# Performance work log

Measured on AMD Instinct MI355X. Metric: run time of the kernel, lower is better.

The kernel has to match this reference:

```python
import jax, jax.numpy as jnp
import numpy as np

N_NODES = 50000
N_EDGES = 800000
D_IN, D_HID, N_CLS, N_PROT = 128, 256, 16, 512
EPS = 1e-6


def setup_inputs() -> dict:
    key = jax.random.key(0)
    ks = jax.random.split(key, 12)
    s = 0.05
    return {
        "x": jax.random.normal(ks[0], (N_NODES, D_IN), dtype=jnp.float32),
        "edge_index": jax.random.randint(ks[1], (2, N_EDGES), 0, N_NODES, dtype=jnp.int64),
        "prot": jax.random.randint(ks[2], (N_PROT,), 0, N_NODES, dtype=jnp.int64),
        "epoch": 1,
        "W0": jax.random.normal(ks[3], (D_IN, D_HID), dtype=jnp.float32) * s,
        "b0": jnp.zeros((D_HID,), jnp.float32),
        "W1": jax.random.normal(ks[4], (D_HID, D_HID), dtype=jnp.float32) * s,
        "b1": jnp.zeros((D_HID,), jnp.float32),
        "Wl1": jax.random.normal(ks[5], (D_HID, D_HID), dtype=jnp.float32) * s,
        "bl1": jnp.zeros((D_HID,), jnp.float32),
        "Wl2": jax.random.normal(ks[6], (D_HID, N_CLS), dtype=jnp.float32) * s,
        "bl2": jnp.zeros((N_CLS,), jnp.float32),
    }


def _gcn_layer(h, W, b, src, dst, norm, n):
    # PyG GCNConv: h' = scatter_add(norm * (h @ W)[src] -> dst) + b
    m = (h @ W)[src] * norm[:, None]
    return jax.ops.segment_sum(m, dst, num_segments=n) + b


def _forward(x, edge_index, prot, W0, b0, W1, b1, Wl1, bl1, Wl2, bl2):
    n = x.shape[0]
    loops = jnp.arange(n, dtype=edge_index.dtype)
    src = jnp.concatenate([edge_index[0], loops])
    dst = jnp.concatenate([edge_index[1], loops])
    deg = jax.ops.segment_sum(jnp.ones_like(dst, dtype=x.dtype), dst, num_segments=n)
    dis = jax.lax.rsqrt(deg)  # deg >= 1 thanks to self loops
    norm = dis[src] * dis[dst]

    h = jax.nn.relu(_gcn_layer(x, W0, b0, src, dst, norm, n))
    h = _gcn_layer(h, W1, b1, src, dst, norm, n)

    # L2 row-normalize (torch divides by the norm directly)
    qn = jnp.linalg.norm(h, axis=1, keepdims=True)
    h = h / qn

    # relative_rep: cosine similarity of every node to each anchor
    anchors = h[prot]                             # [P, H]
    nx = jnp.linalg.norm(h, axis=1)               # [N]
    na = jnp.linalg.norm(anchors, axis=1)         # [P]
    num = h @ anchors.T                           # [N, P]
    x_rel = num / jnp.maximum(nx[:, None] * na[None, :], EPS)

    # classifier head on prototypes -> out_proto, then composed prediction
    lin = lambda z: jax.nn.relu(z @ Wl1 + bl1) @ Wl2 + bl2
    out_proto = jax.nn.log_softmax(lin(anchors), axis=-1)   # [P, C]
    out = jax.nn.log_softmax(x_rel @ out_proto, axis=-1)    # [N, C]
    return out, x_rel, out_proto


def reference(x, edge_index, prot, epoch, W0, b0, W1, b1, Wl1, bl1, Wl2, bl2):
    # epoch >= first_step_epochs (=0) branch: inference-path composition
    return _forward(x, edge_index, prot, W0, b0, W1, b1, Wl1, bl1, Wl2, bl2)


if __name__ == "__main__":
    out, x_rel, out_proto = reference(**setup_inputs())
    print(out.shape, x_rel.shape, out_proto.shape)
```

## Files before the change

kernel.cpp:

```cpp
#include <hip/hip_runtime.h>
#include <hip/hip_bf16.h>
#include <math.h>

#define NN 50000
#define NP 50048
#define EE 800000
#define DIN 128
#define HID 256
#define NCLS 16
#define NPROT 512

typedef __attribute__((ext_vector_type(8))) short short8;
typedef __attribute__((ext_vector_type(4))) float f32x4;

__device__ inline unsigned short f2b(float f) {
    union { float f; unsigned u; } c; c.f = f;
    unsigned u = c.u;
    unsigned r = (u + 0x7FFFu + ((u >> 16) & 1u)) >> 16;
    return (unsigned short)r;
}
__device__ inline float b2f(unsigned short u) {
    union { unsigned u; float f; } c; c.u = ((unsigned)u) << 16; return c.f;
}

#define GL2LDS16(g, l)                                                              \
    __builtin_amdgcn_global_load_lds(                                               \
        (const __attribute__((address_space(1))) unsigned int*)(g),                 \
        (__attribute__((address_space(3))) unsigned int*)(l), 16, 0, 0)


__global__ __launch_bounds__(256) void k_count(const int* __restrict__ dst, int* __restrict__ cnt, int e) {
    int i = blockIdx.x * 256 + threadIdx.x;
    if (i < e) atomicAdd(&cnt[dst[i]], 1);
}

__global__ __launch_bounds__(256) void k_scan1(const int* __restrict__ cnt, int* __restrict__ excl,
                                               int* __restrict__ bsum, float* __restrict__ dis, int n) {
    __shared__ int s[256];
    int t = threadIdx.x;
    int i = blockIdx.x * 256 + t;
    int v = (i < n) ? cnt[i] : 0;
    if (i < n) dis[i] = rsqrtf((float)v + 1.0f);
    s[t] = v; __syncthreads();
    for (int d = 1; d < 256; d <<= 1) {
        int add = (t >= d) ? s[t - d] : 0;
        __syncthreads();
        s[t] += add;
        __syncthreads();
    }
    if (i < n) excl[i] = s[t] - v;
    if (t == 255) bsum[blockIdx.x] = s[255];
}

__global__ __launch_bounds__(256) void k_scan2(const int* __restrict__ bsum, int* __restrict__ boff, int nb) {
    __shared__ int s[256];
    int t = threadIdx.x;
    int v = (t < nb) ? bsum[t] : 0;
    s[t] = v; __syncthreads();
    for (int d = 1; d < 256; d <<= 1) {
        int add = (t >= d) ? s[t - d] : 0;
        __syncthreads();
        s[t] += add;
        __syncthreads();
    }
    if (t < nb) boff[t] = s[t] - v;
}

__global__ __launch_bounds__(256) void k_scan3(const int* __restrict__ excl, const int* __restrict__ boff,
                                               int* __restrict__ off, int n, int e) {
    int i = blockIdx.x * 256 + threadIdx.x;
    if (i < n) off[i] = excl[i] + boff[blockIdx.x];
    if (i == 0) off[n] = e;
}

__global__ __launch_bounds__(256) void k_fill(const int* __restrict__ src, const int* __restrict__ dst,
                                              const int* __restrict__ off, int* __restrict__ cursor,
                                              const float* __restrict__ dis,
                                              int2* __restrict__ csr_e, int e) {
    int i = blockIdx.x * 256 + threadIdx.x;
    if (i >= e) return;
    int s = src[i], d = dst[i];
    int pos = atomicAdd(&cursor[d], 1);
    csr_e[off[d] + pos] = make_int2(s, __float_as_int(dis[s] * dis[d]));
}


#define CAST_BLKS (NN * DIN / 4 / 256)
#define WT0_BLKS  (DIN * HID / 256)
#define WT1_BLKS  (HID * HID / 256)

__global__ __launch_bounds__(256) void k_prep(const float* __restrict__ x, unsigned short* __restrict__ xb,
                                              const float* __restrict__ W0, unsigned short* __restrict__ Wt0,
                                              const float* __restrict__ W1, unsigned short* __restrict__ Wt1) {
    int b = blockIdx.x, t = threadIdx.x;
    if (b < CAST_BLKS) {
        int i = b * 256 + t;
        float4 v = ((const float4*)x)[i];
        ushort4 o; o.x = f2b(v.x); o.y = f2b(v.y); o.z = f2b(v.z); o.w = f2b(v.w);
        ((ushort4*)xb)[i] = o;
    } else if (b < CAST_BLKS + WT0_BLKS) {
        int i = (b - CAST_BLKS) * 256 + t;
        int k = i / HID, n = i - k * HID;
        Wt0[n * DIN + k] = f2b(W0[(size_t)k * HID + n]);
    } else {
        int i = (b - CAST_BLKS - WT0_BLKS) * 256 + t;
        int k = i / HID, n = i - k * HID;
        Wt1[n * HID + k] = f2b(W1[(size_t)k * HID + n]);
    }
}


__global__ __launch_bounds__(256) void k_gemm_mfma(const unsigned short* __restrict__ A,
                                                   const unsigned short* __restrict__ Bt,
                                                   void* __restrict__ C, int M, int Nc, int K, int mode,
                                                   const float* __restrict__ nx, const float* __restrict__ na,
                                                   const float* __restrict__ bias) {
    __shared__ __align__(16) unsigned short As[128 * 32];
    __shared__ __align__(16) unsigned short Bs[128 * 32];
    const int t = threadIdx.x;
    const int lane = t & 63;
    const int quad = lane >> 4;
    const int l16 = lane & 15;
    const int wv = t >> 6;
    const int wm = (wv & 1) * 64, wn = (wv >> 1) * 64;
    const int m0 = blockIdx.y * 128, n0 = blockIdx.x * 128;

    f32x4 acc[4][4];
#pragma unroll
    for (int i = 0; i < 4; ++i)
#pragma unroll
        for (int j = 0; j < 4; ++j)
#pragma unroll
            for (int r = 0; r < 4; ++r) acc[i][j][r] = 0.0f;

    const int sr = t >> 2;
    const int sc = (t & 3) * 8;

    for (int k0 = 0; k0 < K; k0 += 32) {
        GL2LDS16(A + (size_t)(m0 + sr) * K + k0 + sc,       &As[t * 8]);
        GL2LDS16(A + (size_t)(m0 + 64 + sr) * K + k0 + sc,  &As[2048 + t * 8]);
        GL2LDS16(Bt + (size_t)(n0 + sr) * K + k0 + sc,      &Bs[t * 8]);
        GL2LDS16(Bt + (size_t)(n0 + 64 + sr) * K + k0 + sc, &Bs[2048 + t * 8]);
        __syncthreads();
        short8 af[4], bf[4];
#pragma unroll
        for (int i = 0; i < 4; ++i)
            af[i] = *(const short8*)&As[(wm + i * 16 + l16) * 32 + quad * 8];
#pragma unroll
        for (int j = 0; j < 4; ++j)
            bf[j] = *(const short8*)&Bs[(wn + j * 16 + l16) * 32 + quad * 8];
#pragma unroll
        for (int i = 0; i < 4; ++i)
#pragma unroll
            for (int j = 0; j < 4; ++j)
                acc[i][j] = __builtin_amdgcn_mfma_f32_16x16x32_bf16(af[i], bf[j], acc[i][j], 0, 0, 0);
        __syncthreads();
    }

#pragma unroll
    for (int i = 0; i < 4; ++i) {
        int rb = m0 + wm + i * 16 + quad * 4;
#pragma unroll
        for (int j = 0; j < 4; ++j) {
            int col = n0 + wn + j * 16 + l16;
#pragma unroll
            for (int rg = 0; rg < 4; ++rg) {
                int r = rb + rg;
                float v = acc[i][j][rg];
                if (mode == 0) {
                    ((unsigned short*)C)[(size_t)r * Nc + col] = f2b(v);
                } else if (mode == 2) {
                    v = fmaxf(v + bias[col], 0.0f);
                    ((unsigned short*)C)[(size_t)r * Nc + col] = f2b(v);
                } else if (r < M) {
                    float s = fmaxf(nx[r] * na[col], 1e-6f);
                    ((float*)C)[(size_t)r * Nc + col] = v / s;
                }
            }
        }
    }
}


__global__ __launch_bounds__(256) void k_agg128(const unsigned short* __restrict__ xw, const int* __restrict__ off,
                                                const int2* __restrict__ csr, const float* __restrict__ dis,
                                                unsigned short* __restrict__ out, int n) {
    int node = (blockIdx.x * 256 + threadIdx.x) >> 6;
    int lane = threadIdx.x & 63;
    if (node >= n) return;
    float d = dis[node];
    float w0 = d * d;
    ushort2 u = ((const ushort2*)(xw + (size_t)node * DIN))[lane];
    float a0 = w0 * b2f(u.x), a1 = w0 * b2f(u.y);
    int p = off[node], p1 = off[node + 1];
#define G128(e)                                                           \
    {                                                                     \
        ushort2 v = ((const ushort2*)(xw + (size_t)(e).x * DIN))[lane];   \
        float w = __int_as_float((e).y);                                  \
        a0 = fmaf(w, b2f(v.x), a0); a1 = fmaf(w, b2f(v.y), a1);           \
    }
    for (; p + 3 < p1; p += 4) {
        int2 e0 = csr[p], e1 = csr[p + 1], e2 = csr[p + 2], e3 = csr[p + 3];
        G128(e0) G128(e1) G128(e2) G128(e3)
    }
    for (; p < p1; ++p) { int2 e0 = csr[p]; G128(e0) }
#undef G128
    ushort2 o; o.x = f2b(a0); o.y = f2b(a1);
    ((ushort2*)(out + (size_t)node * DIN))[lane] = o;
}


__global__ __launch_bounds__(256) void k_agg256(const unsigned short* __restrict__ xw, const int* __restrict__ off,
                                                const int2* __restrict__ csr, const float* __restrict__ dis,
                                                const float* __restrict__ bias,
                                                unsigned short* __restrict__ out, float* __restrict__ nx, int n) {
    int node = (blockIdx.x * 256 + threadIdx.x) >> 6;
    int lane = threadIdx.x & 63;
    if (node >= n) return;
    float d = dis[node];
    float w0 = d * d;
    ushort4 u = ((const ushort4*)(xw + (size_t)node * HID))[lane];
    float a0 = w0 * b2f(u.x), a1 = w0 * b2f(u.y), a2 = w0 * b2f(u.z), a3 = w0 * b2f(u.w);
    int p = off[node], p1 = off[node + 1];
#define G256(e)                                                           \
    {                                                                     \
        ushort4 v = ((const ushort4*)(xw + (size_t)(e).x * HID))[lane];   \
        float w = __int_as_float((e).y);                                  \
        a0 = fmaf(w, b2f(v.x), a0); a1 = fmaf(w, b2f(v.y), a1);           \
        a2 = fmaf(w, b2f(v.z), a2); a3 = fmaf(w, b2f(v.w), a3);           \
    }
    for (; p + 3 < p1; p += 4) {
        int2 e0 = csr[p], e1 = csr[p + 1], e2 = csr[p + 2], e3 = csr[p + 3];
        G256(e0) G256(e1) G256(e2) G256(e3)
    }
    for (; p < p1; ++p) { int2 e0 = csr[p]; G256(e0) }
#undef G256
    float4 b = ((const float4*)bias)[lane];
    a0 += b.x; a1 += b.y; a2 += b.z; a3 += b.w;
    float ss = a0 * a0 + a1 * a1 + a2 * a2 + a3 * a3;
    for (int m = 32; m >= 1; m >>= 1) ss += __shfl_xor(ss, m, 64);
    float qn = sqrtf(ss);
    a0 /= qn; a1 /= qn; a2 /= qn; a3 /= qn;
    float s2 = a0 * a0 + a1 * a1 + a2 * a2 + a3 * a3;
    for (int m = 32; m >= 1; m >>= 1) s2 += __shfl_xor(s2, m, 64);
    if (lane == 0) nx[node] = sqrtf(s2);
    ushort4 o; o.x = f2b(a0); o.y = f2b(a1); o.z = f2b(a2); o.w = f2b(a3);
    ((ushort4*)(out + (size_t)node * HID))[lane] = o;
}


__global__ __launch_bounds__(256) void k_gproto(const unsigned short* __restrict__ hb,
                                                const int* __restrict__ prot, const float* __restrict__ nx,
                                                unsigned short* __restrict__ aRb, float* __restrict__ na,
                                                const float* __restrict__ Wl1, const float* __restrict__ bl1,
                                                const float* __restrict__ Wl2, const float* __restrict__ bl2,
                                                float* __restrict__ outp) {
    __shared__ float sa[HID];
    __shared__ float st[HID];
    int row = blockIdx.x, t = threadIdx.x;
    int p = prot[row];
    unsigned short us = hb[(size_t)p * HID + t];
    aRb[(size_t)row * HID + t] = us;
    sa[t] = b2f(us);
    if (t == 0) na[row] = nx[p];
    __syncthreads();
    float acc = bl1[t];
#pragma unroll 8
    for (int k = 0; k < HID; ++k) acc = fmaf(sa[k], Wl1[k * HID + t], acc);
    st[t] = fmaxf(acc, 0.0f);
    __syncthreads();
    if (t < 64) {
        int c = t & 15, ch = t >> 4;
        float z = 0.f;
#pragma unroll 8
        for (int k = ch * 64; k < ch * 64 + 64; ++k) z = fmaf(st[k], Wl2[k * NCLS + c], z);
        z += __shfl_xor(z, 16, 64);
        z += __shfl_xor(z, 32, 64);
        z += bl2[c];
        float m = z;
        for (int d = 8; d >= 1; d >>= 1) m = fmaxf(m, __shfl_xor(m, d, 64));
        float e = expf(z - m);
        float s = e;
        for (int d = 8; d >= 1; d >>= 1) s += __shfl_xor(s, d, 64);
        if (t < 16) outp[row * NCLS + c] = z - m - logf(s);
    }
}


__global__ __launch_bounds__(256) void k_final(const float* __restrict__ xrel, const float* __restrict__ proto,
                                               float* __restrict__ out, int M) {
    __shared__ __align__(16) unsigned short pT[16 * 520];
    int t = threadIdx.x;
    for (int i = t; i < NPROT * NCLS; i += 256) {
        int k = i >> 4, c = i & 15;
        pT[c * 520 + k] = f2b(proto[i]);
    }
    __syncthreads();
    const int lane = t & 63, wv = t >> 6;
    const int quad = lane >> 4, l16 = lane & 15;
    short8 bfr[16];
#pragma unroll
    for (int ks = 0; ks < 16; ++ks)
        bfr[ks] = *(const short8*)&pT[l16 * 520 + ks * 32 + quad * 8];
    int m0 = blockIdx.x * 128;
#pragma unroll
    for (int mt = 0; mt < 2; ++mt) {
        int tile0 = m0 + (wv * 2 + mt) * 16;
        int r = tile0 + l16;
        int rl = (r < M) ? r : (M - 1);
        const float* xr = xrel + (size_t)rl * NPROT + quad * 8;
        f32x4 acc = {0.f, 0.f, 0.f, 0.f};
#pragma unroll
        for (int ks = 0; ks < 16; ++ks) {
            float4 v0 = *(const float4*)(xr + ks * 32);
            float4 v1 = *(const float4*)(xr + ks * 32 + 4);
            short8 af;
            af[0] = (short)f2b(v0.x); af[1] = (short)f2b(v0.y);
            af[2] = (short)f2b(v0.z); af[3] = (short)f2b(v0.w);
            af[4] = (short)f2b(v1.x); af[5] = (short)f2b(v1.y);
            af[6] = (short)f2b(v1.z); af[7] = (short)f2b(v1.w);
            acc = __builtin_amdgcn_mfma_f32_16x16x32_bf16(af, bfr[ks], acc, 0, 0, 0);
        }
#pragma unroll
        for (int rg = 0; rg < 4; ++rg) {
            int row = tile0 + quad * 4 + rg;
            float z = acc[rg];
            float mx = z;
            for (int d = 8; d >= 1; d >>= 1) mx = fmaxf(mx, __shfl_xor(mx, d, 64));
            float e = expf(z - mx);
            float s = e;
            for (int d = 8; d >= 1; d >>= 1) s += __shfl_xor(s, d, 64);
            if (row < M) out[(size_t)row * NCLS + l16] = z - mx - logf(s);
        }
    }
}


extern "C" void kernel_launch(void* const* d_in, const int* in_sizes, int n_in,
                              void* d_out, int out_size, void* d_ws, size_t ws_size,
                              hipStream_t stream) {
    const float* x    = (const float*)d_in[0];
    const int*   eidx = (const int*)d_in[1];
    const int*   prot = (const int*)d_in[2];
    const float* W0  = (const float*)d_in[4];
    const float* b0  = (const float*)d_in[5];
    const float* W1  = (const float*)d_in[6];
    const float* b1  = (const float*)d_in[7];
    const float* Wl1 = (const float*)d_in[8];
    const float* bl1 = (const float*)d_in[9];
    const float* Wl2 = (const float*)d_in[10];
    const float* bl2 = (const float*)d_in[11];

    const int N = NN, E = EE;
    const int* esrc_in = eidx;
    const int* edst_in = eidx + E;

    float* out_final = (float*)d_out;
    float* x_rel     = (float*)d_out + (size_t)N * NCLS;
    float* out_proto = x_rel + (size_t)N * NPROT;

    char* w = (char*)d_ws;
    auto alloc = [&](size_t bytes) { char* p = w; w += (bytes + 255) & ~(size_t)255; return p; };
    int*   cnt      = (int*)alloc((size_t)N * 4);
    int*   cursor   = (int*)alloc((size_t)N * 4);
    float* dis      = (float*)alloc((size_t)N * 4);
    int*   excl     = (int*)alloc((size_t)N * 4);
    int*   csr_off  = (int*)alloc((size_t)(N + 1) * 4);
    int*   bsum     = (int*)alloc(1024);
    int*   boff     = (int*)alloc(1024);
    int2*  csr_e    = (int2*)alloc((size_t)E * 8);
    float* nx       = (float*)alloc((size_t)N * 4);
    float* na       = (float*)alloc((size_t)NPROT * 4);
    unsigned short* xb    = (unsigned short*)alloc((size_t)NP * DIN * 2);
    unsigned short* Wt0   = (unsigned short*)alloc((size_t)HID * DIN * 2);
    unsigned short* Wt1   = (unsigned short*)alloc((size_t)HID * HID * 2);
    unsigned short* bufAb = (unsigned short*)alloc((size_t)NP * HID * 2);
    unsigned short* h0b   = (unsigned short*)alloc((size_t)NP * HID * 2);
    unsigned short* aRb   = (unsigned short*)alloc((size_t)NPROT * HID * 2);
    unsigned short* a1 = bufAb;
    unsigned short* hb = h0b;

    hipMemsetAsync(cnt, 0, (size_t)N * 4, stream);
    hipMemsetAsync(cursor, 0, (size_t)N * 4, stream);

    k_count<<<(E + 255) / 256, 256, 0, stream>>>(edst_in, cnt, E);
    int NB = (N + 255) / 256;
    k_scan1<<<NB, 256, 0, stream>>>(cnt, excl, bsum, dis, N);
    k_scan2<<<1, 256, 0, stream>>>(bsum, boff, NB);
    k_scan3<<<NB, 256, 0, stream>>>(excl, boff, csr_off, N, E);
    k_fill<<<(E + 255) / 256, 256, 0, stream>>>(esrc_in, edst_in, csr_off, cursor, dis, csr_e, E);

    k_prep<<<CAST_BLKS + WT0_BLKS + WT1_BLKS, 256, 0, stream>>>(x, xb, W0, Wt0, W1, Wt1);

    const int MT = NP / 128;

    k_agg128<<<(N + 3) / 4, 256, 0, stream>>>(xb, csr_off, csr_e, dis, a1, N);
    k_gemm_mfma<<<dim3(HID / 128, MT), 256, 0, stream>>>(a1, Wt0, h0b, N, HID, DIN, 2, nullptr, nullptr, b0);

    k_gemm_mfma<<<dim3(HID / 128, MT), 256, 0, stream>>>(h0b, Wt1, bufAb, N, HID, HID, 0, nullptr, nullptr, nullptr);
    k_agg256<<<(N + 3) / 4, 256, 0, stream>>>(bufAb, csr_off, csr_e, dis, b1, hb, nx, N);

    k_gproto<<<NPROT, 256, 0, stream>>>(hb, prot, nx, aRb, na, Wl1, bl1, Wl2, bl2, out_proto);

    k_gemm_mfma<<<dim3(NPROT / 128, MT), 256, 0, stream>>>(hb, aRb, x_rel, N, NPROT, HID, 1, nx, na, nullptr);

    k_final<<<MT, 256, 0, stream>>>(x_rel, out_proto, out_final, N);
}
```

Baseline: 490.8 us.

## Fuse x_rel GEMM with final prototype projection and log-softmax

The x_rel cosine-similarity GEMM and the final x_rel @ out_proto + log_softmax are merged into one kernel. Each block loops over all 512 prototype columns, stages the normalized tile in LDS as bf16, writes x_rel out, and accumulates the 16-class logits with MFMA. This removes the round trip that read x_rel back from global memory in a second kernel. In exchange, x_rel is now stored after a bf16 round trip, which loses precision, and each block now does four times the work with far fewer blocks in flight.

```diff
diff --git a/kernel.cpp b/kernel.cpp
--- a/kernel.cpp
+++ b/kernel.cpp
@@ -113,7 +113,6 @@
 __global__ __launch_bounds__(256) void k_gemm_mfma(const unsigned short* __restrict__ A,
                                                    const unsigned short* __restrict__ Bt,
                                                    void* __restrict__ C, int M, int Nc, int K, int mode,
-                                                   const float* __restrict__ nx, const float* __restrict__ na,
                                                    const float* __restrict__ bias) {
     __shared__ __align__(16) unsigned short As[128 * 32];
     __shared__ __align__(16) unsigned short Bs[128 * 32];
@@ -169,12 +168,9 @@
                 float v = acc[i][j][rg];
                 if (mode == 0) {
                     ((unsigned short*)C)[(size_t)r * Nc + col] = f2b(v);
-                } else if (mode == 2) {
+                } else {
                     v = fmaxf(v + bias[col], 0.0f);
                     ((unsigned short*)C)[(size_t)r * Nc + col] = f2b(v);
-                } else if (r < M) {
-                    float s = fmaxf(nx[r] * na[col], 1e-6f);
-                    ((float*)C)[(size_t)r * Nc + col] = v / s;
                 }
             }
         }
@@ -287,50 +283,139 @@
 }
 
 
-__global__ __launch_bounds__(256) void k_final(const float* __restrict__ xrel, const float* __restrict__ proto,
-                                               float* __restrict__ out, int M) {
-    __shared__ __align__(16) unsigned short pT[16 * 520];
-    int t = threadIdx.x;
-    for (int i = t; i < NPROT * NCLS; i += 256) {
-        int k = i >> 4, c = i & 15;
-        pT[c * 520 + k] = f2b(proto[i]);
-    }
-    __syncthreads();
-    const int lane = t & 63, wv = t >> 6;
-    const int quad = lane >> 4, l16 = lane & 15;
-    short8 bfr[16];
-#pragma unroll
-    for (int ks = 0; ks < 16; ++ks)
-        bfr[ks] = *(const short8*)&pT[l16 * 520 + ks * 32 + quad * 8];
-    int m0 = blockIdx.x * 128;
-#pragma unroll
-    for (int mt = 0; mt < 2; ++mt) {
-        int tile0 = m0 + (wv * 2 + mt) * 16;
-        int r = tile0 + l16;
-        int rl = (r < M) ? r : (M - 1);
-        const float* xr = xrel + (size_t)rl * NPROT + quad * 8;
-        f32x4 acc = {0.f, 0.f, 0.f, 0.f};
-#pragma unroll
-        for (int ks = 0; ks < 16; ++ks) {
-            float4 v0 = *(const float4*)(xr + ks * 32);
-            float4 v1 = *(const float4*)(xr + ks * 32 + 4);
-            short8 af;
-            af[0] = (short)f2b(v0.x); af[1] = (short)f2b(v0.y);
-            af[2] = (short)f2b(v0.z); af[3] = (short)f2b(v0.w);
-            af[4] = (short)f2b(v1.x); af[5] = (short)f2b(v1.y);
-            af[6] = (short)f2b(v1.z); af[7] = (short)f2b(v1.w);
-            acc = __builtin_amdgcn_mfma_f32_16x16x32_bf16(af, bfr[ks], acc, 0, 0, 0);
-        }
+#define XST 136
+
+__global__ __launch_bounds__(256) void k_xrel_out(const unsigned short* __restrict__ A,
+                                                  const unsigned short* __restrict__ Bt,
+                                                  const float* __restrict__ nx, const float* __restrict__ na,
+                                                  const float* __restrict__ proto,
+                                                  float* __restrict__ xrel, float* __restrict__ out) {
+    __shared__ __align__(16) unsigned short As[128 * 32];
+    __shared__ __align__(16) unsigned short Bs[128 * 32];
+    __shared__ __align__(16) unsigned short Xs[128 * XST];
+    __shared__ __align__(16) unsigned short pTc[16 * XST];
+
+    const int t = threadIdx.x;
+    const int lane = t & 63;
+    const int quad = lane >> 4;
+    const int l16 = lane & 15;
+    const int wv = t >> 6;
+    const int wm = (wv & 1) * 64, wn = (wv >> 1) * 64;
+    const int m0 = blockIdx.x * 128;
+
+    float nxv[4][4];
+#pragma unroll
+    for (int i = 0; i < 4; ++i)
 #pragma unroll
         for (int rg = 0; rg < 4; ++rg) {
-            int row = tile0 + quad * 4 + rg;
-            float z = acc[rg];
+            int r = m0 + wm + i * 16 + quad * 4 + rg;
+            nxv[i][rg] = nx[r < NN ? r : NN - 1];
+        }
+
+    const int sr = t >> 2;
+    const int sc = (t & 3) * 8;
+
+    f32x4 oacc[2];
+#pragma unroll
+    for (int r = 0; r < 4; ++r) { oacc[0][r] = 0.0f; oacc[1][r] = 0.0f; }
+
+    for (int n0 = 0; n0 < NPROT; n0 += 128) {
+        f32x4 acc[4][4];
+#pragma unroll
+        for (int i = 0; i < 4; ++i)
+#pragma unroll
+            for (int j = 0; j < 4; ++j)
+#pragma unroll
+                for (int r = 0; r < 4; ++r) acc[i][j][r] = 0.0f;
+
+        for (int k0 = 0; k0 < HID; k0 += 32) {
+            GL2LDS16(A + (size_t)(m0 + sr) * HID + k0 + sc,       &As[t * 8]);
+            GL2LDS16(A + (size_t)(m0 + 64 + sr) * HID + k0 + sc,  &As[2048 + t * 8]);
+            GL2LDS16(Bt + (size_t)(n0 + sr) * HID + k0 + sc,      &Bs[t * 8]);
+            GL2LDS16(Bt + (size_t)(n0 + 64 + sr) * HID + k0 + sc, &Bs[2048 + t * 8]);
+            __syncthreads();
+            short8 af[4], bf[4];
+#pragma unroll
+            for (int i = 0; i < 4; ++i)
+                af[i] = *(const short8*)&As[(wm + i * 16 + l16) * 32 + quad * 8];
+#pragma unroll
+            for (int j = 0; j < 4; ++j)
+                bf[j] = *(const short8*)&Bs[(wn + j * 16 + l16) * 32 + quad * 8];
+#pragma unroll
+            for (int i = 0; i < 4; ++i)
+#pragma unroll
+                for (int j = 0; j < 4; ++j)
+                    acc[i][j] = __builtin_amdgcn_mfma_f32_16x16x32_bf16(af[i], bf[j], acc[i][j], 0, 0, 0);
+            __syncthreads();
+        }
+
+        for (int i = t; i < 128 * NCLS; i += 256) {
+            int kk = i >> 4, c = i & 15;
+            pTc[c * XST + kk] = f2b(proto[(n0 + kk) * NCLS + c]);
+        }
+
+        float nav[4];
+#pragma unroll
+        for (int j = 0; j < 4; ++j) nav[j] = na[n0 + wn + j * 16 + l16];
+#pragma unroll
+        for (int i = 0; i < 4; ++i) {
+            int rls = (wm + i * 16 + quad * 4) * XST;
+#pragma unroll
+            for (int j = 0; j < 4; ++j) {
+                int cl = wn + j * 16 + l16;
+#pragma unroll
+                for (int rg = 0; rg < 4; ++rg) {
+                    float s = fmaxf(nxv[i][rg] * nav[j], 1e-6f);
+                    float v = acc[i][j][rg] * __builtin_amdgcn_rcpf(s);
+                    Xs[rls + rg * XST + cl] = f2b(v);
+                }
+            }
+        }
+        __syncthreads();
+
+#pragma unroll
+        for (int ii = 0; ii < 2; ++ii) {
+            int rb = wv * 32 + ii * 16;
+#pragma unroll
+            for (int ks = 0; ks < 4; ++ks) {
+                short8 af = *(const short8*)&Xs[(rb + l16) * XST + ks * 32 + quad * 8];
+                short8 pb = *(const short8*)&pTc[l16 * XST + ks * 32 + quad * 8];
+                oacc[ii] = __builtin_amdgcn_mfma_f32_16x16x32_bf16(af, pb, oacc[ii], 0, 0, 0);
+            }
+        }
+
+#pragma unroll
+        for (int it = 0; it < 8; ++it) {
+            int idx = it * 256 + t;
+            int row = idx >> 4;
+            int c8 = (idx & 15) * 8;
+            int r = m0 + row;
+            if (r < NN) {
+                short8 u = *(const short8*)&Xs[row * XST + c8];
+                float* dst = &xrel[(size_t)r * NPROT + n0 + c8];
+                float4 v0, v1;
+                v0.x = b2f((unsigned short)u[0]); v0.y = b2f((unsigned short)u[1]);
+                v0.z = b2f((unsigned short)u[2]); v0.w = b2f((unsigned short)u[3]);
+                v1.x = b2f((unsigned short)u[4]); v1.y = b2f((unsigned short)u[5]);
+                v1.z = b2f((unsigned short)u[6]); v1.w = b2f((unsigned short)u[7]);
+                *(float4*)dst = v0;
+                *(float4*)(dst + 4) = v1;
+            }
+        }
+    }
+
+#pragma unroll
+    for (int ii = 0; ii < 2; ++ii) {
+#pragma unroll
+        for (int rg = 0; rg < 4; ++rg) {
+            int row = m0 + wv * 32 + ii * 16 + quad * 4 + rg;
+            float z = oacc[ii][rg];
             float mx = z;
             for (int d = 8; d >= 1; d >>= 1) mx = fmaxf(mx, __shfl_xor(mx, d, 64));
             float e = expf(z - mx);
-            float s = e;
-            for (int d = 8; d >= 1; d >>= 1) s += __shfl_xor(s, d, 64);
-            if (row < M) out[(size_t)row * NCLS + l16] = z - mx - logf(s);
+            float ssum = e;
+            for (int d = 8; d >= 1; d >>= 1) ssum += __shfl_xor(ssum, d, 64);
+            if (row < NN) out[(size_t)row * NCLS + l16] = z - mx - logf(ssum);
         }
     }
 }
@@ -395,14 +480,12 @@
     const int MT = NP / 128;
 
     k_agg128<<<(N + 3) / 4, 256, 0, stream>>>(xb, csr_off, csr_e, dis, a1, N);
-    k_gemm_mfma<<<dim3(HID / 128, MT), 256, 0, stream>>>(a1, Wt0, h0b, N, HID, DIN, 2, nullptr, nullptr, b0);
-
-    k_gemm_mfma<<<dim3(HID / 128, MT), 256, 0, stream>>>(h0b, Wt1, bufAb, N, HID, HID, 0, nullptr, nullptr, nullptr);
+    k_gemm_mfma<<<dim3(HID / 128, MT), 256, 0, stream>>>(a1, Wt0, h0b, N, HID, DIN, 2, b0);
+
+    k_gemm_mfma<<<dim3(HID / 128, MT), 256, 0, stream>>>(h0b, Wt1, bufAb, N, HID, HID, 0, nullptr);
     k_agg256<<<(N + 3) / 4, 256, 0, stream>>>(bufAb, csr_off, csr_e, dis, b1, hb, nx, N);
 
     k_gproto<<<NPROT, 256, 0, stream>>>(hb, prot, nx, aRb, na, Wl1, bl1, Wl2, bl2, out_proto);
 
-    k_gemm_mfma<<<dim3(NPROT / 128, MT), 256, 0, stream>>>(hb, aRb, x_rel, N, NPROT, HID, 1, nx, na, nullptr);
-
-    k_final<<<MT, 256, 0, stream>>>(x_rel, out_proto, out_final, N);
-}
+    k_xrel_out<<<MT, 256, 0, stream>>>(hb, aRb, nx, na, out_proto, x_rel, out_final);
+}
```

Result: faster. 479.4 us (-2.3%).
